# Performance work log

Hardware: AMD Instinct MI355X
Metric: run time of the kernel (lower is better)

Reference implementation:

```python
import jax, jax.numpy as jnp
import numpy as np

B, SEQ, DIM, D, K = 32, 2048, 512, 512, 128


def _ln(x, g, b, eps=1e-5):
    m = x.mean(-1, keepdims=True)
    v = ((x - m) ** 2).mean(-1, keepdims=True)
    return (x - m) / jnp.sqrt(v + eps) * g + b


def _gelu(v):
    return jax.nn.gelu(v, approximate=False)


def _diff_topk(s, k, t):
    # s: (B, N) scores; iterative relaxed top-k (Xie & Ermon style).
    def step(carry, _):
        a = jax.nn.softmax(carry / t, axis=-1)
        carry = carry + jnp.log(jnp.clip(1.0 - a, 1e-6, 1.0))
        return carry, a
    _, Ws = jax.lax.scan(step, s, None, length=k)  # (k, B, N)
    return jnp.transpose(Ws, (1, 0, 2))            # (B, k, N)


def setup_inputs():
    key = jax.random.key(0)
    ks = jax.random.split(key, 6)
    w = lambda k_, shape: jax.random.normal(k_, shape, dtype=jnp.float32) * 0.02
    return {
        'x': jax.random.normal(ks[0], (B, SEQ, DIM), dtype=jnp.float32),
        'tau': jnp.array(0.0, dtype=jnp.float32),
        'ln1_g': jnp.ones((DIM,), jnp.float32), 'ln1_b': jnp.zeros((DIM,), jnp.float32),
        'W1': w(ks[1], (DIM, D)), 'b1': jnp.zeros((D,), jnp.float32),
        'ln2_g': jnp.ones((SEQ,), jnp.float32), 'ln2_b': jnp.zeros((SEQ,), jnp.float32),
        'W2': w(ks[2], (SEQ, SEQ)), 'b2': jnp.zeros((SEQ,), jnp.float32),
        'ln3_g': jnp.ones((D,), jnp.float32), 'ln3_b': jnp.zeros((D,), jnp.float32),
        'W3': w(ks[3], (D, D + 1)), 'b3': jnp.zeros((D + 1,), jnp.float32),
        'ln4_g': jnp.ones((D,), jnp.float32), 'ln4_b': jnp.zeros((D,), jnp.float32),
        'W4': w(ks[4], (D, DIM)), 'b4': jnp.zeros((DIM,), jnp.float32),
    }


def reference(x, tau, ln1_g, ln1_b, W1, b1, ln2_g, ln2_b, W2, b2,
              ln3_g, ln3_b, W3, b3, ln4_g, ln4_b, W4, b4):
    # tok_proj: LN(dim) -> Linear(dim, D) -> GELU
    x_tok = _gelu(_ln(x, ln1_g, ln1_b) @ W1 + b1)                  # (B, N, D)
    # ch_proj over the token axis: LN(seq) -> Linear(seq, seq) -> GELU
    xt = jnp.swapaxes(x_tok, 1, 2)                                  # (B, D, N)
    x_ch = jnp.swapaxes(_gelu(_ln(xt, ln2_g, ln2_b) @ W2 + b2), 1, 2)
    # proj -> split score | features
    h = _ln(x_tok + x_ch, ln3_g, ln3_b) @ W3 + b3                   # (B, N, D+1)
    x_score, x_proj = h[..., 0], h[..., 1:]
    t = jax.nn.sigmoid(jnp.clip(tau, -2.0, 5.0))
    Wmat = _diff_topk(x_score, K, t)                                # (B, k, N)
    Z = jnp.einsum('bkn,bnd->bkd', Wmat, x_proj)                    # soft gather
    Y = jnp.einsum('bkn,bkd->bnd', Wmat, Z)                         # soft scatter
    return _ln(x_proj + Y, ln4_g, ln4_b) @ W4 + b4                  # (B, N, dim)
```

## Files before the change

kernel.cpp:

```cpp
#include <hip/hip_runtime.h>
#include <math.h>

#define B_   32
#define SEQ_ 2048
#define DIM_ 512
#define KSEL 128

typedef _Float16 f16;
typedef _Float16 half8 __attribute__((ext_vector_type(8)));
typedef _Float16 half4 __attribute__((ext_vector_type(4)));
typedef float floatx4 __attribute__((ext_vector_type(4)));

#define LSTR2 32

__device__ __forceinline__ float gelu_exact(float v) {
  return 0.5f * v * (1.0f + erff(v * 0.70710678118654752440f));
}

__global__ __launch_bounds__(256) void ln_fuse_f32(const float* __restrict__ X,
    const float* __restrict__ g, const float* __restrict__ bl,
    f16* __restrict__ Y) {
  int row = blockIdx.x * 4 + (threadIdx.x >> 6);
  int l = threadIdx.x & 63;
  const float4* p = (const float4*)(X + (size_t)row * 512);
  float4 v0 = p[l * 2], v1 = p[l * 2 + 1];
  float s = v0.x + v0.y + v0.z + v0.w + v1.x + v1.y + v1.z + v1.w;
  float q = v0.x*v0.x + v0.y*v0.y + v0.z*v0.z + v0.w*v0.w
          + v1.x*v1.x + v1.y*v1.y + v1.z*v1.z + v1.w*v1.w;
#pragma unroll
  for (int off = 32; off > 0; off >>= 1) {
    s += __shfl_xor(s, off);
    q += __shfl_xor(q, off);
  }
  float m = s * (1.0f / 512.0f);
  float sd = rsqrtf(q * (1.0f / 512.0f) - m * m + 1e-5f);
  float4 g0 = ((const float4*)(g + l * 8))[0];
  float4 g1v = ((const float4*)(g + l * 8))[1];
  float4 b0 = ((const float4*)(bl + l * 8))[0];
  float4 b1v = ((const float4*)(bl + l * 8))[1];
  half8 o;
  o[0] = (f16)((v0.x - m) * sd * g0.x + b0.x);
  o[1] = (f16)((v0.y - m) * sd * g0.y + b0.y);
  o[2] = (f16)((v0.z - m) * sd * g0.z + b0.z);
  o[3] = (f16)((v0.w - m) * sd * g0.w + b0.w);
  o[4] = (f16)((v1.x - m) * sd * g1v.x + b1v.x);
  o[5] = (f16)((v1.y - m) * sd * g1v.y + b1v.y);
  o[6] = (f16)((v1.z - m) * sd * g1v.z + b1v.z);
  o[7] = (f16)((v1.w - m) * sd * g1v.w + b1v.w);
  *(half8*)(Y + (size_t)row * 512 + l * 8) = o;
}

__global__ __launch_bounds__(256) void ln_fuse_f16(const f16* __restrict__ X,
    const float* __restrict__ g, const float* __restrict__ bl,
    f16* __restrict__ Y) {
  int row = blockIdx.x * 4 + (threadIdx.x >> 6);
  int l = threadIdx.x & 63;
  half8 h = *(const half8*)(X + (size_t)row * 512 + l * 8);
  float v[8];
  float s = 0.f, q = 0.f;
#pragma unroll
  for (int i = 0; i < 8; ++i) { v[i] = (float)h[i]; s += v[i]; q += v[i] * v[i]; }
#pragma unroll
  for (int off = 32; off > 0; off >>= 1) {
    s += __shfl_xor(s, off);
    q += __shfl_xor(q, off);
  }
  float m = s * (1.0f / 512.0f);
  float sd = rsqrtf(q * (1.0f / 512.0f) - m * m + 1e-5f);
  float4 g0 = ((const float4*)(g + l * 8))[0];
  float4 g1v = ((const float4*)(g + l * 8))[1];
  float4 b0 = ((const float4*)(bl + l * 8))[0];
  float4 b1v = ((const float4*)(bl + l * 8))[1];
  half8 o;
  o[0] = (f16)((v[0] - m) * sd * g0.x + b0.x);
  o[1] = (f16)((v[1] - m) * sd * g0.y + b0.y);
  o[2] = (f16)((v[2] - m) * sd * g0.z + b0.z);
  o[3] = (f16)((v[3] - m) * sd * g0.w + b0.w);
  o[4] = (f16)((v[4] - m) * sd * g1v.x + b1v.x);
  o[5] = (f16)((v[5] - m) * sd * g1v.y + b1v.y);
  o[6] = (f16)((v[6] - m) * sd * g1v.z + b1v.z);
  o[7] = (f16)((v[7] - m) * sd * g1v.w + b1v.w);
  *(half8*)(Y + (size_t)row * 512 + l * 8) = o;
}

__global__ __launch_bounds__(256) void rowstats_score(const f16* __restrict__ X,
    const float* __restrict__ g3, const float* __restrict__ bl3,
    const f16* __restrict__ w3c , const float* __restrict__ b3,
    float* __restrict__ mean, float* __restrict__ rstd,
    float* __restrict__ xscore) {
  int row = blockIdx.x * 4 + (threadIdx.x >> 6);
  int l = threadIdx.x & 63;
  half8 h = *(const half8*)(X + (size_t)row * 512 + l * 8);
  float v[8];
  float s = 0.f, q = 0.f;
#pragma unroll
  for (int i = 0; i < 8; ++i) { v[i] = (float)h[i]; s += v[i]; q += v[i] * v[i]; }
#pragma unroll
  for (int off = 32; off > 0; off >>= 1) {
    s += __shfl_xor(s, off);
    q += __shfl_xor(q, off);
  }
  float m = s * (1.0f / 512.0f);
  float sd = rsqrtf(q * (1.0f / 512.0f) - m * m + 1e-5f);
  half8 wv = *(const half8*)(w3c + l * 8);
  float4 g0 = ((const float4*)(g3 + l * 8))[0];
  float4 g1v = ((const float4*)(g3 + l * 8))[1];
  float4 b0 = ((const float4*)(bl3 + l * 8))[0];
  float4 b1v = ((const float4*)(bl3 + l * 8))[1];
  float gv[8] = {g0.x, g0.y, g0.z, g0.w, g1v.x, g1v.y, g1v.z, g1v.w};
  float bv[8] = {b0.x, b0.y, b0.z, b0.w, b1v.x, b1v.y, b1v.z, b1v.w};
  float dot = 0.f;
#pragma unroll
  for (int i = 0; i < 8; ++i)
    dot += ((v[i] - m) * sd * gv[i] + bv[i]) * (float)wv[i];
#pragma unroll
  for (int off = 32; off > 0; off >>= 1) dot += __shfl_xor(dot, off);
  if (l == 0) {
    mean[row] = m;
    rstd[row] = sd;
    xscore[row] = dot + b3[0];
  }
}

__global__ __launch_bounds__(512) void colstats_part(const f16* __restrict__ xtok,
                                                     float2* __restrict__ part) {
  int b = blockIdx.x >> 3, pr = blockIdx.x & 7;
  int d = threadIdx.x;
  const f16* src = xtok + ((size_t)b * SEQ_ + (size_t)pr * 256) * 512 + d;
  float s = 0.f, q = 0.f;
#pragma unroll 4
  for (int i = 0; i < 256; ++i) {
    float v = (float)src[(size_t)i * 512];
    s += v; q += v * v;
  }
  part[(size_t)blockIdx.x * 512 + d] = make_float2(s, q);
}

__global__ __launch_bounds__(256) void colstats_fin(const float2* __restrict__ part,
                                                    float* __restrict__ mean,
                                                    float* __restrict__ rstd) {
  int idx = blockIdx.x * 256 + threadIdx.x;
  int b = idx >> 9;
  float s = 0.f, q = 0.f;
#pragma unroll
  for (int p = 0; p < 8; ++p) {
    float2 v = part[((size_t)(b * 8 + p)) * 512 + (idx & 511)];
    s += v.x; q += v.y;
  }
  float m = s * (1.0f / 2048.0f);
  mean[idx] = m;
  rstd[idx] = rsqrtf(q * (1.0f / 2048.0f) - m * m + 1e-5f);
}

template <typename T>
__global__ __launch_bounds__(256) void transpose_cvt(const T* __restrict__ src,
                                                     f16* __restrict__ dst,
                                                     int R, int C, long sb, long db) {
  __shared__ float tile[32][33];
  const T* s = src + (long)blockIdx.z * sb;
  f16* d = dst + (long)blockIdx.z * db;
  int c0 = blockIdx.x * 32, r0 = blockIdx.y * 32;
  int tx = threadIdx.x, ty = threadIdx.y;
#pragma unroll
  for (int i = 0; i < 4; ++i) {
    int r = r0 + ty + i * 8, c = c0 + tx;
    if (r < R && c < C) tile[ty + i * 8][tx] = (float)s[(long)r * C + c];
  }
  __syncthreads();
#pragma unroll
  for (int i = 0; i < 4; ++i) {
    int c = c0 + ty + i * 8, r = r0 + tx;
    if (c < C && r < R) d[(long)c * R + r] = (f16)tile[tx][ty + i * 8];
  }
}

__global__ __launch_bounds__(256) void trans2_kernel(const f16* __restrict__ xtok,
    const float* __restrict__ mean2, const float* __restrict__ rstd2,
    const float* __restrict__ g2, const float* __restrict__ bl2,
    f16* __restrict__ A2) {
  __shared__ float tile[32][33];
  int b = blockIdx.z;
  const f16* src = xtok + (long)b * SEQ_ * 512;
  f16* dst = A2 + (long)b * 512 * SEQ_;
  int d0 = blockIdx.x * 32, s0 = blockIdx.y * 32;
  int tx = threadIdx.x, ty = threadIdx.y;
  float m = mean2[b * 512 + d0 + tx];
  float rs = rstd2[b * 512 + d0 + tx];
#pragma unroll
  for (int i = 0; i < 4; ++i) {
    int s = s0 + ty + i * 8;
    float v = (float)src[(long)s * 512 + d0 + tx];
    tile[ty + i * 8][tx] = (v - m) * rs * g2[s] + bl2[s];
  }
  __syncthreads();
#pragma unroll
  for (int i = 0; i < 4; ++i) {
    int d = d0 + ty + i * 8, s = s0 + tx;
    dst[(long)d * SEQ_ + s] = (f16)tile[tx][ty + i * 8];
  }
}

__device__ __forceinline__ void stage_gll(const f16* __restrict__ src, long ld,
                                          int row0, int k0, f16* S, int t) {
  int w = t >> 6, lane = t & 63;
  int r = lane >> 2, c8 = (lane & 3) * 8;
#pragma unroll
  for (int i = 0; i < 2; ++i) {
    int chunk = w * 2 + i;
    const f16* g = src + (long)(row0 + chunk * 16 + r) * ld + k0 + c8;
    f16* l = S + chunk * 16 * LSTR2;
    __builtin_amdgcn_global_load_lds(
        (const __attribute__((address_space(1))) void*)g,
        (__attribute__((address_space(3))) void*)l, 16, 0, 0);
  }
}

__device__ __forceinline__ void stage_a_ln_f16(const f16* __restrict__ src, long ld,
    const float* __restrict__ mean, const float* __restrict__ rstd,
    const float* __restrict__ g, const float* __restrict__ bl,
    int row0, int k0, f16* S, int t) {
  int row = t >> 1, kc = (t & 1) * 16;
  int r = row0 + row, c = k0 + kc;
  float m = mean[r], sd = rstd[r];
  const f16* p = src + (long)r * ld + c;
  half8 h0 = *(const half8*)(p);
  half8 h1 = *(const half8*)(p + 8);
  float gv[16], bv[16];
#pragma unroll
  for (int i = 0; i < 4; ++i) {
    float4 gq = ((const float4*)(g + c))[i];
    gv[i*4+0]=gq.x; gv[i*4+1]=gq.y; gv[i*4+2]=gq.z; gv[i*4+3]=gq.w;
    float4 bq = ((const float4*)(bl + c))[i];
    bv[i*4+0]=bq.x; bv[i*4+1]=bq.y; bv[i*4+2]=bq.z; bv[i*4+3]=bq.w;
  }
  half8 o0, o1;
#pragma unroll
  for (int i = 0; i < 8; ++i) {
    o0[i] = (f16)(((float)h0[i] - m) * sd * gv[i] + bv[i]);
    o1[i] = (f16)(((float)h1[i] - m) * sd * gv[i + 8] + bv[i + 8]);
  }
  *(half8*)(S + row * LSTR2 + kc) = o0;
  *(half8*)(S + row * LSTR2 + kc + 8) = o1;
}

__device__ __forceinline__ void mfma_step(const f16* As, const f16* Bs, int lane,
                                          int wr, int wc, floatx4 acc[4][4]) {
  int kc = (lane >> 4) * 8;
  int rl = lane & 15;
  half8 a[4], b[4];
#pragma unroll
  for (int mi = 0; mi < 4; ++mi)
    a[mi] = *(const half8*)(As + (wr * 64 + mi * 16 + rl) * LSTR2 + kc);
#pragma unroll
  for (int ni = 0; ni < 4; ++ni)
    b[ni] = *(const half8*)(Bs + (wc * 64 + ni * 16 + rl) * LSTR2 + kc);
#pragma unroll
  for (int mi = 0; mi < 4; ++mi)
#pragma unroll
    for (int ni = 0; ni < 4; ++ni)
      acc[mi][ni] = __builtin_amdgcn_mfma_f32_16x16x32_f16(a[mi], b[ni], acc[mi][ni], 0, 0, 0);
}

#define GEMM_PROLOG \
  __shared__ __attribute__((aligned(16))) f16 As[128 * LSTR2]; \
  __shared__ __attribute__((aligned(16))) f16 Bs[128 * LSTR2]; \
  int t = threadIdx.x; \
  int lane = t & 63, w = t >> 6, wr = w >> 1, wc = w & 1; \
  floatx4 acc[4][4]; \
  _Pragma("unroll") for (int mi = 0; mi < 4; ++mi) \
  _Pragma("unroll") for (int ni = 0; ni < 4; ++ni) acc[mi][ni] = (floatx4){0.f,0.f,0.f,0.f};

__global__ __launch_bounds__(256) void g1_kernel(const f16* __restrict__ xln1,
    const f16* __restrict__ W1T, const float* __restrict__ b1,
    f16* __restrict__ xtok) {
  GEMM_PROLOG
  int m0 = blockIdx.y * 128, n0 = blockIdx.x * 128;
  for (int k0 = 0; k0 < 512; k0 += 32) {
    stage_gll(xln1, 512, m0, k0, As, t);
    stage_gll(W1T, 512, n0, k0, Bs, t);
    __syncthreads();
    mfma_step(As, Bs, lane, wr, wc, acc);
    __syncthreads();
  }
#pragma unroll
  for (int mi = 0; mi < 4; ++mi)
#pragma unroll
    for (int ni = 0; ni < 4; ++ni) {
      int c = n0 + wc * 64 + ni * 16 + (lane & 15);
      float bias = b1[c];
      int r0 = m0 + wr * 64 + mi * 16 + (lane >> 4) * 4;
#pragma unroll
      for (int j = 0; j < 4; ++j)
        xtok[(long)(r0 + j) * 512 + c] = (f16)gelu_exact(acc[mi][ni][j] + bias);
    }
}

__device__ __forceinline__ void stage_half(const f16* __restrict__ srcbase, long ld,
                                           f16* dst, int tid) {
#pragma unroll
  for (int q = 0; q < 2; ++q) {
    int row = q * 128 + (tid >> 2);
    int slot = (tid & 3) ^ ((row >> 1) & 3);
    const f16* g = srcbase + (long)row * ld + slot * 8;
    f16* lp = dst + (long)(q * 128 + (tid >> 6) * 16) * 32;
    __builtin_amdgcn_global_load_lds(
        (const __attribute__((address_space(1))) void*)g,
        (__attribute__((address_space(3))) void*)lp, 16, 0, 0);
  }
}

__device__ __forceinline__ half8 frag32(const f16* buf, int row, int sl) {
  return *(const half8*)(buf + (long)row * 32 + ((sl ^ ((row >> 1) & 3)) << 3));
}

#define BAR() __builtin_amdgcn_s_barrier()
#define WAITBAR4() do { asm volatile("s_waitcnt vmcnt(4)" ::: "memory"); \
                        __builtin_amdgcn_s_barrier(); } while (0)

__global__ __launch_bounds__(512, 2) void g2_8p(const f16* __restrict__ W2T,
    const f16* __restrict__ A2, const float* __restrict__ b2,
    const f16* __restrict__ xtok, f16* __restrict__ xsum) {
  __shared__ __attribute__((aligned(16))) f16 Ah[2][2][256 * 32];
  __shared__ __attribute__((aligned(16))) f16 Bh[2][2][256 * 32];
  int tid = threadIdx.x;
  int l = tid & 63, w = tid >> 6;
  int wr = w >> 2, wc = w & 3;
  int rl = l & 15, sl = l >> 4;
  int b = blockIdx.y;
  int m0 = blockIdx.z * 256;
  int n0 = blockIdx.x * 256;
  const f16* Am = W2T + (long)m0 * SEQ_;
  const f16* Bm = A2 + (long)b * 512 * SEQ_ + (long)n0 * SEQ_;
  const f16* xtb = xtok + (long)b * SEQ_ * 512;
  f16* xsb = xsum + (long)b * SEQ_ * 512;

  floatx4 acc[8][4];
#pragma unroll
  for (int mf = 0; mf < 8; ++mf)
#pragma unroll
    for (int nf = 0; nf < 4; ++nf) acc[mf][nf] = (floatx4){0.f, 0.f, 0.f, 0.f};

  half8 afr[4], bfr[4];

#define STAGE(base, tile, kk, dstbuf) \
  stage_half(base + (long)((tile) & 31) * 64 + (kk) * 32, SEQ_, dstbuf, tid)

#define READ_B(d, kk) \
  _Pragma("unroll") for (int nf = 0; nf < 4; ++nf) \
    bfr[nf] = frag32(Bh[d][kk], wc * 64 + nf * 16 + rl, sl);

#define READ_A(d, kk, mb) \
  _Pragma("unroll") for (int mi = 0; mi < 4; ++mi) \
    afr[mi] = frag32(Ah[d][kk], wr * 128 + ((mb) + mi) * 16 + rl, sl);

#define MFMA16(mb) \
  __builtin_amdgcn_s_setprio(1); \
  _Pragma("unroll") for (int mi = 0; mi < 4; ++mi) \
  _Pragma("unroll") for (int nf = 0; nf < 4; ++nf) \
    acc[(mb) + mi][nf] = __builtin_amdgcn_mfma_f32_16x16x32_f16(afr[mi], bfr[nf], acc[(mb) + mi][nf], 0, 0, 0); \
  __builtin_amdgcn_s_setprio(0);

  STAGE(Am, 0, 0, Ah[0][0]); STAGE(Am, 0, 1, Ah[0][1]);
  STAGE(Bm, 0, 0, Bh[0][0]); STAGE(Bm, 0, 1, Bh[0][1]);
  STAGE(Am, 1, 0, Ah[1][0]); STAGE(Bm, 1, 0, Bh[1][0]);
  asm volatile("s_waitcnt vmcnt(0)" ::: "memory");
  __builtin_amdgcn_s_barrier();

  for (int i = 0; i < 16; ++i) {
    STAGE(Am, 2 * i + 1, 1, Ah[1][1]);
    READ_B(0, 0); READ_A(0, 0, 0);
    BAR(); MFMA16(0); BAR();
    STAGE(Bm, 2 * i + 1, 1, Bh[1][1]);
    READ_A(0, 0, 4);
    BAR(); MFMA16(4); BAR();
    STAGE(Am, 2 * i + 2, 0, Ah[0][0]);
    READ_B(0, 1); READ_A(0, 1, 0);
    BAR(); MFMA16(0); BAR();
    STAGE(Bm, 2 * i + 2, 0, Bh[0][0]);
    READ_A(0, 1, 4);
    BAR(); MFMA16(4); WAITBAR4();
    STAGE(Am, 2 * i + 2, 1, Ah[0][1]);
    READ_B(1, 0); READ_A(1, 0, 0);
    BAR(); MFMA16(0); BAR();
    STAGE(Bm, 2 * i + 2, 1, Bh[0][1]);
    READ_A(1, 0, 4);
    BAR(); MFMA16(4); BAR();
    STAGE(Am, 2 * i + 3, 0, Ah[1][0]);
    READ_B(1, 1); READ_A(1, 1, 0);
    BAR(); MFMA16(0); BAR();
    STAGE(Bm, 2 * i + 3, 0, Bh[1][0]);
    READ_A(1, 1, 4);
    BAR(); MFMA16(4); WAITBAR4();
  }

#pragma unroll
  for (int mf = 0; mf < 8; ++mf) {
    int rbase = m0 + wr * 128 + mf * 16 + sl * 4;
#pragma unroll
    for (int j = 0; j < 4; ++j) {
      int r = rbase + j;
      float bias = b2[r];
      long rowoff = (long)r * 512;
#pragma unroll
      for (int nf = 0; nf < 4; ++nf) {
        int cc = n0 + wc * 64 + nf * 16 + rl;
        float v = gelu_exact(acc[mf][nf][j] + bias);
        xsb[rowoff + cc] = (f16)((float)xtb[rowoff + cc] + v);
      }
    }
  }
#undef STAGE
#undef READ_B
#undef READ_A
#undef MFMA16
}

__global__ __launch_bounds__(256) void g3_kernel(const f16* __restrict__ xsum,
    const float* __restrict__ mean, const float* __restrict__ rstd,
    const float* __restrict__ g3, const float* __restrict__ bl3,
    const f16* __restrict__ BT , const float* __restrict__ b3,
    f16* __restrict__ xproj, f16* __restrict__ xprojT) {
  GEMM_PROLOG
  int m0 = blockIdx.y * 128, n0 = blockIdx.x * 128;
  for (int k0 = 0; k0 < 512; k0 += 32) {
    stage_a_ln_f16(xsum, 512, mean, rstd, g3, bl3, m0, k0, As, t);
    stage_gll(BT, 512, n0, k0, Bs, t);
    __syncthreads();
    mfma_step(As, Bs, lane, wr, wc, acc);
    __syncthreads();
  }
#pragma unroll
  for (int mi = 0; mi < 4; ++mi)
#pragma unroll
    for (int ni = 0; ni < 4; ++ni) {
      int c = n0 + wc * 64 + ni * 16 + (lane & 15);
      float bias = b3[c + 1];
      int r0 = m0 + wr * 64 + mi * 16 + (lane >> 4) * 4;
      half4 xp;
#pragma unroll
      for (int j = 0; j < 4; ++j) {
        f16 v = (f16)(acc[mi][ni][j] + bias);
        xproj[(long)(r0 + j) * 512 + c] = v;
        xp[j] = v;
      }
      long bb = r0 >> 11;
      long rloc = r0 & 2047;
      *(half4*)(xprojT + (bb * 512 + c) * SEQ_ + rloc) = xp;
    }
}

__global__ __launch_bounds__(512) void topk_kernel(const float* __restrict__ xscore,
                                                   const float* __restrict__ tau,
                                                   f16* __restrict__ Wm) {
  int b = blockIdx.x, t = threadIdx.x;
  __shared__ float red[2][8];
  float tv = fminf(fmaxf(tau[0], -2.0f), 5.0f);
  float temp = 1.0f / (1.0f + __expf(-tv));
  float it = 1.0f / temp;
  float c[4];
  const float* xs = xscore + (size_t)b * SEQ_;
  {
    float4 v = *(const float4*)(xs + t * 4);
    c[0] = v.x; c[1] = v.y; c[2] = v.z; c[3] = v.w;
  }
  int l = t & 63, wid = t >> 6;
  for (int k = 0; k < KSEL; ++k) {
    float e[4];
    float p = 0.f;
#pragma unroll
    for (int i = 0; i < 4; ++i) { e[i] = __expf(c[i] * it); p += e[i]; }
#pragma unroll
    for (int off = 32; off > 0; off >>= 1) p += __shfl_down(p, off);
    if (l == 0) red[k & 1][wid] = p;
    __syncthreads();
    float S = 0.f;
#pragma unroll
    for (int q = 0; q < 8; ++q) S += red[k & 1][q];
    float iS = 1.0f / S;
    half4 h;
    float a[4];
#pragma unroll
    for (int i = 0; i < 4; ++i) { a[i] = e[i] * iS; h[i] = (f16)a[i]; }
    *(half4*)(Wm + ((size_t)b * KSEL + k) * SEQ_ + t * 4) = h;
#pragma unroll
    for (int i = 0; i < 4; ++i) c[i] += __logf(fmaxf(1.0f - a[i], 1e-6f));
  }
}

__global__ __launch_bounds__(256) void gz_kernel(const f16* __restrict__ Wm,
    const f16* __restrict__ xprojT, float* __restrict__ Zpart) {
  GEMM_PROLOG
  int b = blockIdx.z, kc = blockIdx.y;
  int n0 = blockIdx.x * 128;
  const f16* A = Wm + (long)b * KSEL * SEQ_;
  const f16* BT = xprojT + (long)b * 512 * SEQ_;
  float* Zb = Zpart + ((long)b * 2 + kc) * KSEL * 512;
  int kbeg = kc * 1024, kend = kbeg + 1024;
  for (int k0 = kbeg; k0 < kend; k0 += 32) {
    stage_gll(A, SEQ_, 0, k0, As, t);
    stage_gll(BT, SEQ_, n0, k0, Bs, t);
    __syncthreads();
    mfma_step(As, Bs, lane, wr, wc, acc);
    __syncthreads();
  }
#pragma unroll
  for (int mi = 0; mi < 4; ++mi)
#pragma unroll
    for (int ni = 0; ni < 4; ++ni) {
      int c = n0 + wc * 64 + ni * 16 + (lane & 15);
      int r0 = wr * 64 + mi * 16 + (lane >> 4) * 4;
#pragma unroll
      for (int j = 0; j < 4; ++j)
        Zb[(long)(r0 + j) * 512 + c] = acc[mi][ni][j];
    }
}

__global__ __launch_bounds__(256) void ztrans_kernel(const float* __restrict__ Zpart,
                                                     f16* __restrict__ ZT) {
  __shared__ float tile[32][33];
  int b = blockIdx.z;
  int c0 = blockIdx.x * 32, r0 = blockIdx.y * 32;
  int tx = threadIdx.x, ty = threadIdx.y;
  const float* p0 = Zpart + ((long)b * 2 + 0) * KSEL * 512;
  const float* p1 = Zpart + ((long)b * 2 + 1) * KSEL * 512;
#pragma unroll
  for (int i = 0; i < 4; ++i) {
    int r = r0 + ty + i * 8, c = c0 + tx;
    tile[ty + i * 8][tx] = p0[(long)r * 512 + c] + p1[(long)r * 512 + c];
  }
  __syncthreads();
  f16* d = ZT + (long)b * 512 * KSEL;
#pragma unroll
  for (int i = 0; i < 4; ++i) {
    int c = c0 + ty + i * 8, r = r0 + tx;
    d[(long)c * KSEL + r] = (f16)tile[tx][ty + i * 8];
  }
}

__global__ __launch_bounds__(256) void gy_kernel(const f16* __restrict__ WmT,
    const f16* __restrict__ ZT, const f16* __restrict__ xproj,
    f16* __restrict__ rbuf) {
  GEMM_PROLOG
  int b = blockIdx.z;
  int m0 = blockIdx.y * 128, n0 = blockIdx.x * 128;
  const f16* A = WmT + (long)b * SEQ_ * KSEL;
  const f16* BT = ZT + (long)b * 512 * KSEL;
  const f16* xpb = xproj + (long)b * SEQ_ * 512;
  f16* rb = rbuf + (long)b * SEQ_ * 512;
  for (int k0 = 0; k0 < KSEL; k0 += 32) {
    stage_gll(A, KSEL, m0, k0, As, t);
    stage_gll(BT, KSEL, n0, k0, Bs, t);
    __syncthreads();
    mfma_step(As, Bs, lane, wr, wc, acc);
    __syncthreads();
  }
#pragma unroll
  for (int mi = 0; mi < 4; ++mi)
#pragma unroll
    for (int ni = 0; ni < 4; ++ni) {
      int c = n0 + wc * 64 + ni * 16 + (lane & 15);
      int r0 = m0 + wr * 64 + mi * 16 + (lane >> 4) * 4;
#pragma unroll
      for (int j = 0; j < 4; ++j) {
        long idx = (long)(r0 + j) * 512 + c;
        rb[idx] = (f16)((float)xpb[idx] + acc[mi][ni][j]);
      }
    }
}

__global__ __launch_bounds__(256) void g4_kernel(const f16* __restrict__ xln4,
    const f16* __restrict__ W4T, const float* __restrict__ b4,
    float* __restrict__ out) {
  GEMM_PROLOG
  int m0 = blockIdx.y * 128, n0 = blockIdx.x * 128;
  for (int k0 = 0; k0 < 512; k0 += 32) {
    stage_gll(xln4, 512, m0, k0, As, t);
    stage_gll(W4T, 512, n0, k0, Bs, t);
    __syncthreads();
    mfma_step(As, Bs, lane, wr, wc, acc);
    __syncthreads();
  }
#pragma unroll
  for (int mi = 0; mi < 4; ++mi)
#pragma unroll
    for (int ni = 0; ni < 4; ++ni) {
      int c = n0 + wc * 64 + ni * 16 + (lane & 15);
      float bias = b4[c];
      int r0 = m0 + wr * 64 + mi * 16 + (lane >> 4) * 4;
#pragma unroll
      for (int j = 0; j < 4; ++j)
        out[(long)(r0 + j) * 512 + c] = acc[mi][ni][j] + bias;
    }
}

extern "C" void kernel_launch(void* const* d_in, const int* in_sizes, int n_in,
                              void* d_out, int out_size, void* d_ws, size_t ws_size,
                              hipStream_t stream) {
  const float* x    = (const float*)d_in[0];
  const float* tau  = (const float*)d_in[1];
  const float* g1   = (const float*)d_in[2];
  const float* bl1  = (const float*)d_in[3];
  const float* W1   = (const float*)d_in[4];
  const float* b1   = (const float*)d_in[5];
  const float* g2   = (const float*)d_in[6];
  const float* bl2  = (const float*)d_in[7];
  const float* W2   = (const float*)d_in[8];
  const float* b2   = (const float*)d_in[9];
  const float* g3   = (const float*)d_in[10];
  const float* bl3  = (const float*)d_in[11];
  const float* W3   = (const float*)d_in[12];
  const float* b3   = (const float*)d_in[13];
  const float* g4   = (const float*)d_in[14];
  const float* bl4  = (const float*)d_in[15];
  const float* W4   = (const float*)d_in[16];
  const float* b4   = (const float*)d_in[17];
  float* out = (float*)d_out;

  const long NTOK = (long)B_ * SEQ_;

  char* ws = (char*)d_ws;
  f16* regA   = (f16*)(ws);
  f16* regB   = (f16*)(ws + (64l << 20));
  float* Zpart = (float*)(ws + (128l << 20));
  f16* W2T    = (f16*)(ws + (144l << 20));
  f16* W1T    = (f16*)(ws + (152l << 20));
  f16* W3T    = (f16*)(ws + (153l << 20));
  f16* W4T    = (f16*)(ws + (154l << 20));
  float* xscore = (float*)(ws + (155l << 20));
  float* meanA  = (float*)(ws + (156l << 20));
  float* rstdA  = meanA + NTOK;
  float* mean2  = rstdA + NTOK;
  float* rstd2  = mean2 + B_ * 512;
  float2* part  = (float2*)(rstd2 + B_ * 512);
  f16* ZT     = (f16*)(ws + (157l << 20));

  f16* xtok   = (f16*)d_out;
  f16* xln1   = (f16*)((char*)d_out + (64l << 20));
  f16* xprojT = (f16*)d_out;
  f16* Wm     = (f16*)((char*)d_out + (64l << 20));
  f16* WmT    = (f16*)((char*)d_out + (80l << 20));

  f16* A2    = regA;
  f16* xsum  = regB;
  f16* xproj = regA;
  f16* rbuf  = regB;
  f16* xln4  = regA;

  dim3 tb(32, 8);

  transpose_cvt<float><<<dim3(16, 16, 1), tb, 0, stream>>>(W1, W1T, 512, 512, 0, 0);
  transpose_cvt<float><<<dim3(64, 64, 1), tb, 0, stream>>>(W2, W2T, 2048, 2048, 0, 0);
  transpose_cvt<float><<<dim3(17, 16, 1), tb, 0, stream>>>(W3, W3T, 512, 513, 0, 0);
  transpose_cvt<float><<<dim3(16, 16, 1), tb, 0, stream>>>(W4, W4T, 512, 512, 0, 0);

  ln_fuse_f32<<<NTOK / 4, 256, 0, stream>>>(x, g1, bl1, xln1);
  g1_kernel<<<dim3(4, 512), 256, 0, stream>>>(xln1, W1T, b1, xtok);

  colstats_part<<<B_ * 8, 512, 0, stream>>>(xtok, part);
  colstats_fin<<<64, 256, 0, stream>>>(part, mean2, rstd2);
  trans2_kernel<<<dim3(16, 64, B_), tb, 0, stream>>>(xtok, mean2, rstd2, g2, bl2, A2);
  g2_8p<<<dim3(2, 32, 8), 512, 0, stream>>>(W2T, A2, b2, xtok, xsum);

  rowstats_score<<<NTOK / 4, 256, 0, stream>>>(xsum, g3, bl3, W3T, b3,
                                               meanA, rstdA, xscore);
  g3_kernel<<<dim3(4, 512), 256, 0, stream>>>(xsum, meanA, rstdA, g3, bl3, W3T + 512, b3,
                                              xproj, xprojT);

  topk_kernel<<<B_, 512, 0, stream>>>(xscore, tau, Wm);

  transpose_cvt<f16><<<dim3(64, 4, B_), tb, 0, stream>>>(Wm, WmT, 128, 2048,
      (long)KSEL * SEQ_, (long)SEQ_ * KSEL);

  gz_kernel<<<dim3(4, 2, B_), 256, 0, stream>>>(Wm, xprojT, Zpart);
  ztrans_kernel<<<dim3(16, 4, B_), tb, 0, stream>>>(Zpart, ZT);

  gy_kernel<<<dim3(4, 16, B_), 256, 0, stream>>>(WmT, ZT, xproj, rbuf);

  ln_fuse_f16<<<NTOK / 4, 256, 0, stream>>>(rbuf, g4, bl4, xln4);
  g4_kernel<<<dim3(4, 512), 256, 0, stream>>>(xln4, W4T, b4, out);
}
```

Before: 794.0 us.

## Materialize LN3 output in stats kernel and compute Z transposed directly

```diff
diff --git a/kernel.cpp b/kernel.cpp
--- a/kernel.cpp
+++ b/kernel.cpp
@@ -83,11 +83,10 @@
   *(half8*)(Y + (size_t)row * 512 + l * 8) = o;
 }
 
-__global__ __launch_bounds__(256) void rowstats_score(const f16* __restrict__ X,
+__global__ __launch_bounds__(256) void ln3_fuse_score(const f16* __restrict__ X,
     const float* __restrict__ g3, const float* __restrict__ bl3,
     const f16* __restrict__ w3c , const float* __restrict__ b3,
-    float* __restrict__ mean, float* __restrict__ rstd,
-    float* __restrict__ xscore) {
+    f16* __restrict__ xln3, float* __restrict__ xscore) {
   int row = blockIdx.x * 4 + (threadIdx.x >> 6);
   int l = threadIdx.x & 63;
   half8 h = *(const half8*)(X + (size_t)row * 512 + l * 8);
@@ -110,16 +109,17 @@
   float gv[8] = {g0.x, g0.y, g0.z, g0.w, g1v.x, g1v.y, g1v.z, g1v.w};
   float bv[8] = {b0.x, b0.y, b0.z, b0.w, b1v.x, b1v.y, b1v.z, b1v.w};
   float dot = 0.f;
-#pragma unroll
-  for (int i = 0; i < 8; ++i)
-    dot += ((v[i] - m) * sd * gv[i] + bv[i]) * (float)wv[i];
+  half8 o;
+#pragma unroll
+  for (int i = 0; i < 8; ++i) {
+    float n = (v[i] - m) * sd * gv[i] + bv[i];
+    o[i] = (f16)n;
+    dot += n * (float)wv[i];
+  }
+  *(half8*)(xln3 + (size_t)row * 512 + l * 8) = o;
 #pragma unroll
   for (int off = 32; off > 0; off >>= 1) dot += __shfl_xor(dot, off);
-  if (l == 0) {
-    mean[row] = m;
-    rstd[row] = sd;
-    xscore[row] = dot + b3[0];
-  }
+  if (l == 0) xscore[row] = dot + b3[0];
 }
 
 __global__ __launch_bounds__(512) void colstats_part(const f16* __restrict__ xtok,
@@ -213,34 +213,6 @@
         (const __attribute__((address_space(1))) void*)g,
         (__attribute__((address_space(3))) void*)l, 16, 0, 0);
   }
-}
-
-__device__ __forceinline__ void stage_a_ln_f16(const f16* __restrict__ src, long ld,
-    const float* __restrict__ mean, const float* __restrict__ rstd,
-    const float* __restrict__ g, const float* __restrict__ bl,
-    int row0, int k0, f16* S, int t) {
-  int row = t >> 1, kc = (t & 1) * 16;
-  int r = row0 + row, c = k0 + kc;
-  float m = mean[r], sd = rstd[r];
-  const f16* p = src + (long)r * ld + c;
-  half8 h0 = *(const half8*)(p);
-  half8 h1 = *(const half8*)(p + 8);
-  float gv[16], bv[16];
-#pragma unroll
-  for (int i = 0; i < 4; ++i) {
-    float4 gq = ((const float4*)(g + c))[i];
-    gv[i*4+0]=gq.x; gv[i*4+1]=gq.y; gv[i*4+2]=gq.z; gv[i*4+3]=gq.w;
-    float4 bq = ((const float4*)(bl + c))[i];
-    bv[i*4+0]=bq.x; bv[i*4+1]=bq.y; bv[i*4+2]=bq.z; bv[i*4+3]=bq.w;
-  }
-  half8 o0, o1;
-#pragma unroll
-  for (int i = 0; i < 8; ++i) {
-    o0[i] = (f16)(((float)h0[i] - m) * sd * gv[i] + bv[i]);
-    o1[i] = (f16)(((float)h1[i] - m) * sd * gv[i + 8] + bv[i + 8]);
-  }
-  *(half8*)(S + row * LSTR2 + kc) = o0;
-  *(half8*)(S + row * LSTR2 + kc + 8) = o1;
 }
 
 __device__ __forceinline__ void mfma_step(const f16* As, const f16* Bs, int lane,
@@ -415,15 +387,13 @@
 #undef MFMA16
 }
 
-__global__ __launch_bounds__(256) void g3_kernel(const f16* __restrict__ xsum,
-    const float* __restrict__ mean, const float* __restrict__ rstd,
-    const float* __restrict__ g3, const float* __restrict__ bl3,
+__global__ __launch_bounds__(256) void g3_kernel(const f16* __restrict__ xln3,
     const f16* __restrict__ BT , const float* __restrict__ b3,
     f16* __restrict__ xproj, f16* __restrict__ xprojT) {
   GEMM_PROLOG
   int m0 = blockIdx.y * 128, n0 = blockIdx.x * 128;
   for (int k0 = 0; k0 < 512; k0 += 32) {
-    stage_a_ln_f16(xsum, 512, mean, rstd, g3, bl3, m0, k0, As, t);
+    stage_gll(xln3, 512, m0, k0, As, t);
     stage_gll(BT, 512, n0, k0, Bs, t);
     __syncthreads();
     mfma_step(As, Bs, lane, wr, wc, acc);
@@ -487,18 +457,18 @@
   }
 }
 
-__global__ __launch_bounds__(256) void gz_kernel(const f16* __restrict__ Wm,
-    const f16* __restrict__ xprojT, float* __restrict__ Zpart) {
+__global__ __launch_bounds__(256) void gzt_kernel(const f16* __restrict__ xprojT,
+    const f16* __restrict__ Wm, float* __restrict__ ZTpart) {
   GEMM_PROLOG
   int b = blockIdx.z, kc = blockIdx.y;
-  int n0 = blockIdx.x * 128;
-  const f16* A = Wm + (long)b * KSEL * SEQ_;
-  const f16* BT = xprojT + (long)b * 512 * SEQ_;
-  float* Zb = Zpart + ((long)b * 2 + kc) * KSEL * 512;
+  int m0 = blockIdx.x * 128;
+  const f16* A = xprojT + (long)b * 512 * SEQ_;
+  const f16* Bm = Wm + (long)b * KSEL * SEQ_;
+  float* Zb = ZTpart + ((long)b * 2 + kc) * 512 * KSEL;
   int kbeg = kc * 1024, kend = kbeg + 1024;
   for (int k0 = kbeg; k0 < kend; k0 += 32) {
-    stage_gll(A, SEQ_, 0, k0, As, t);
-    stage_gll(BT, SEQ_, n0, k0, Bs, t);
+    stage_gll(A, SEQ_, m0, k0, As, t);
+    stage_gll(Bm, SEQ_, 0, k0, Bs, t);
     __syncthreads();
     mfma_step(As, Bs, lane, wr, wc, acc);
     __syncthreads();
@@ -507,33 +477,27 @@
   for (int mi = 0; mi < 4; ++mi)
 #pragma unroll
     for (int ni = 0; ni < 4; ++ni) {
-      int c = n0 + wc * 64 + ni * 16 + (lane & 15);
-      int r0 = wr * 64 + mi * 16 + (lane >> 4) * 4;
+      int c = wc * 64 + ni * 16 + (lane & 15);
+      int r0 = m0 + wr * 64 + mi * 16 + (lane >> 4) * 4;
 #pragma unroll
       for (int j = 0; j < 4; ++j)
-        Zb[(long)(r0 + j) * 512 + c] = acc[mi][ni][j];
+        Zb[(long)(r0 + j) * KSEL + c] = acc[mi][ni][j];
     }
 }
 
-__global__ __launch_bounds__(256) void ztrans_kernel(const float* __restrict__ Zpart,
-                                                     f16* __restrict__ ZT) {
-  __shared__ float tile[32][33];
-  int b = blockIdx.z;
-  int c0 = blockIdx.x * 32, r0 = blockIdx.y * 32;
-  int tx = threadIdx.x, ty = threadIdx.y;
-  const float* p0 = Zpart + ((long)b * 2 + 0) * KSEL * 512;
-  const float* p1 = Zpart + ((long)b * 2 + 1) * KSEL * 512;
-#pragma unroll
-  for (int i = 0; i < 4; ++i) {
-    int r = r0 + ty + i * 8, c = c0 + tx;
-    tile[ty + i * 8][tx] = p0[(long)r * 512 + c] + p1[(long)r * 512 + c];
-  }
-  __syncthreads();
+__global__ __launch_bounds__(256) void zred_kernel(const float* __restrict__ ZTpart,
+                                                   f16* __restrict__ ZT) {
+  int b = blockIdx.x;
+  const float* p0 = ZTpart + ((long)b * 2 + 0) * 512 * KSEL;
+  const float* p1 = ZTpart + ((long)b * 2 + 1) * 512 * KSEL;
   f16* d = ZT + (long)b * 512 * KSEL;
-#pragma unroll
-  for (int i = 0; i < 4; ++i) {
-    int c = c0 + ty + i * 8, r = r0 + tx;
-    d[(long)c * KSEL + r] = (f16)tile[tx][ty + i * 8];
+  for (int i = threadIdx.x; i < 512 * KSEL / 4; i += 256) {
+    float4 a = ((const float4*)p0)[i];
+    float4 c = ((const float4*)p1)[i];
+    half4 h;
+    h[0] = (f16)(a.x + c.x); h[1] = (f16)(a.y + c.y);
+    h[2] = (f16)(a.z + c.z); h[3] = (f16)(a.w + c.w);
+    ((half4*)d)[i] = h;
   }
 }
 
@@ -621,21 +585,20 @@
   char* ws = (char*)d_ws;
   f16* regA   = (f16*)(ws);
   f16* regB   = (f16*)(ws + (64l << 20));
-  float* Zpart = (float*)(ws + (128l << 20));
+  float* ZTpart = (float*)(ws + (128l << 20));
   f16* W2T    = (f16*)(ws + (144l << 20));
   f16* W1T    = (f16*)(ws + (152l << 20));
   f16* W3T    = (f16*)(ws + (153l << 20));
   f16* W4T    = (f16*)(ws + (154l << 20));
   float* xscore = (float*)(ws + (155l << 20));
-  float* meanA  = (float*)(ws + (156l << 20));
-  float* rstdA  = meanA + NTOK;
-  float* mean2  = rstdA + NTOK;
+  float* mean2  = (float*)(ws + (156l << 20));
   float* rstd2  = mean2 + B_ * 512;
   float2* part  = (float2*)(rstd2 + B_ * 512);
   f16* ZT     = (f16*)(ws + (157l << 20));
 
   f16* xtok   = (f16*)d_out;
   f16* xln1   = (f16*)((char*)d_out + (64l << 20));
+  f16* xln3   = (f16*)((char*)d_out + (64l << 20));
   f16* xprojT = (f16*)d_out;
   f16* Wm     = (f16*)((char*)d_out + (64l << 20));
   f16* WmT    = (f16*)((char*)d_out + (80l << 20));
@@ -661,18 +624,16 @@
   trans2_kernel<<<dim3(16, 64, B_), tb, 0, stream>>>(xtok, mean2, rstd2, g2, bl2, A2);
   g2_8p<<<dim3(2, 32, 8), 512, 0, stream>>>(W2T, A2, b2, xtok, xsum);
 
-  rowstats_score<<<NTOK / 4, 256, 0, stream>>>(xsum, g3, bl3, W3T, b3,
-                                               meanA, rstdA, xscore);
-  g3_kernel<<<dim3(4, 512), 256, 0, stream>>>(xsum, meanA, rstdA, g3, bl3, W3T + 512, b3,
-                                              xproj, xprojT);
+  ln3_fuse_score<<<NTOK / 4, 256, 0, stream>>>(xsum, g3, bl3, W3T, b3, xln3, xscore);
+  g3_kernel<<<dim3(4, 512), 256, 0, stream>>>(xln3, W3T + 512, b3, xproj, xprojT);
 
   topk_kernel<<<B_, 512, 0, stream>>>(xscore, tau, Wm);
 
   transpose_cvt<f16><<<dim3(64, 4, B_), tb, 0, stream>>>(Wm, WmT, 128, 2048,
       (long)KSEL * SEQ_, (long)SEQ_ * KSEL);
 
-  gz_kernel<<<dim3(4, 2, B_), 256, 0, stream>>>(Wm, xprojT, Zpart);
-  ztrans_kernel<<<dim3(16, 4, B_), tb, 0, stream>>>(Zpart, ZT);
+  gzt_kernel<<<dim3(4, 2, B_), 256, 0, stream>>>(xprojT, Wm, ZTpart);
+  zred_kernel<<<B_, 256, 0, stream>>>(ZTpart, ZT);
 
   gy_kernel<<<dim3(4, 16, B_), 256, 0, stream>>>(WmT, ZT, xproj, rbuf);
 
```

New measurement: 789.4 us. Within noise of the previous version (-0.6%).
